# Kernel tuning notes

Hardware: AMD Instinct MI355X
Metric: run time of the kernel (lower is better)

Reference implementation:

```python
import jax, jax.numpy as jnp
import numpy as np

MAXDISP = 4  # matches init_kwargs


def setup_inputs() -> dict:
    key = jax.random.key(0)
    k1, k2 = jax.random.split(key)
    shape = (4, 64, 64, 128)  # (b, c, H, W)
    return {
        "refimg_fea": jax.random.normal(k1, shape, dtype=jnp.float32),
        "targetimg_fea": jax.random.normal(k2, shape, dtype=jnp.float32),
    }


def _correlation(ref, tgt, md=MAXDISP):
    # cost[b,c,i,j,y,x] = ref[b,c,y,x] * tgt[b,c,y+(j-md), x+(i-md)] when in
    # bounds, else 0 (the torch code pre-fills with zeros). Zero-padding the
    # target reproduces the out-of-bounds zeros exactly, since the product with
    # a padded zero is 0 and leaky_relu(0) == 0.
    b, c, H, W = ref.shape
    D = 2 * md + 1
    tpad = jnp.pad(tgt, ((0, 0), (0, 0), (md, md), (md, md)))

    def shift(i, j):
        # i indexes the width offset (ind), j the height offset (indd),
        # matching cost[:, :, i, j] in the original double loop.
        return jax.lax.dynamic_slice(tpad, (0, 0, j, i), (b, c, H, W))

    idx = jnp.arange(D)
    # shifts: [D_i, D_j, b, c, H, W]
    shifts = jax.vmap(lambda i: jax.vmap(lambda j: shift(i, j))(idx))(idx)
    cost = jax.nn.leaky_relu(ref[None, None] * shifts, negative_slope=0.1)
    # -> (b, c, D_i, D_j, H, W)
    return jnp.transpose(cost, (2, 3, 0, 1, 4, 5))


def reference(refimg_fea, targetimg_fea):
    return _correlation(refimg_fea, targetimg_fea, MAXDISP)
```

## Files before the change

kernel.cpp:

```cpp
#include <hip/hip_runtime.h>

#define MD 4
#define DD 9
#define B  4
#define C  64
#define H  64
#define W  128
#define W4 (W / 4)
#define HW (H * W)

typedef float f32x4 __attribute__((ext_vector_type(4)));


__device__ __forceinline__ float lrelu(float p) {
    return fmaxf(p, 0.1f * p);
}

__global__ __launch_bounds__(256) void corr_kernel(const float* __restrict__ ref,
                                                   const float* __restrict__ tgt,
                                                   float* __restrict__ out) {
    const unsigned bc = blockIdx.x >> 3;
    const unsigned yg = blockIdx.x & 7;
    const unsigned x4 = threadIdx.x & 31;
    const unsigned y  = yg * 8 + (threadIdx.x >> 5);
    const unsigned x  = x4 * 4;

    const f32x4 r = *reinterpret_cast<const f32x4*>(ref + ((size_t)bc * H + y) * W + x);

    float* const out_base = out + (size_t)bc * (DD * DD * HW) + (size_t)y * W + x;
    const float* const tgt_bc = tgt + (size_t)bc * HW;

    #pragma unroll
    for (int j = 0; j < DD; ++j) {
        const int ty = (int)y + j - MD;
        f32x4 tm = {0.f, 0.f, 0.f, 0.f};
        f32x4 tc = {0.f, 0.f, 0.f, 0.f};
        f32x4 tp = {0.f, 0.f, 0.f, 0.f};
        if (ty >= 0 && ty < H) {
            const float* trow = tgt_bc + (size_t)ty * W;
            if (x4 > 0)  tm = *reinterpret_cast<const f32x4*>(trow + x - 4);
            tc = *reinterpret_cast<const f32x4*>(trow + x);
            if (x4 < W4 - 1) tp = *reinterpret_cast<const f32x4*>(trow + x + 4);
        }
        float t[12] = {tm.x, tm.y, tm.z, tm.w,
                       tc.x, tc.y, tc.z, tc.w,
                       tp.x, tp.y, tp.z, tp.w};

        float* op = out_base + (size_t)j * HW;
        #pragma unroll
        for (int i = 0; i < DD; ++i) {
            f32x4 o;
            o.x = lrelu(r.x * t[i + 0]);
            o.y = lrelu(r.y * t[i + 1]);
            o.z = lrelu(r.z * t[i + 2]);
            o.w = lrelu(r.w * t[i + 3]);
            __builtin_nontemporal_store(o, reinterpret_cast<f32x4*>(op));
            op += (size_t)DD * HW;
        }
    }
}

extern "C" void kernel_launch(void* const* d_in, const int* in_sizes, int n_in,
                              void* d_out, int out_size, void* d_ws, size_t ws_size,
                              hipStream_t stream) {
    const float* ref = (const float*)d_in[0];
    const float* tgt = (const float*)d_in[1];
    float* out = (float*)d_out;

    const unsigned blocks = B * C * (H / 8);
    corr_kernel<<<blocks, 256, 0, stream>>>(ref, tgt, out);
}
```

Before: 136.7 us.

## Stage padded target plane in LDS and loop over width offsets per block

Each block now handles one (batch, channel) plane for three width offsets, loading the target plane into a zero-padded LDS tile per offset and reading shifted windows from LDS instead of issuing bounds-checked global loads. Reference rows are held in registers across all offsets. Grid shrinks to 768 blocks, with repeated LDS clearing and barriers between phases, which may reduce parallelism and the overlap of output stores in a write-bound kernel.

```diff
diff --git a/kernel.cpp b/kernel.cpp
--- a/kernel.cpp
+++ b/kernel.cpp
@@ -6,56 +6,84 @@
 #define C  64
 #define H  64
 #define W  128
-#define W4 (W / 4)
 #define HW (H * W)
+
+#define LROW  136
+#define LROWS 72
+#define LDS_F (LROWS * LROW)
 
 typedef float f32x4 __attribute__((ext_vector_type(4)));
 
-
-__device__ __forceinline__ float lrelu(float p) {
-    return fmaxf(p, 0.1f * p);
+__device__ __forceinline__ f32x4 lrelu4(f32x4 p) {
+    f32x4 o;
+    o.x = fmaxf(p.x, 0.1f * p.x);
+    o.y = fmaxf(p.y, 0.1f * p.y);
+    o.z = fmaxf(p.z, 0.1f * p.z);
+    o.w = fmaxf(p.w, 0.1f * p.w);
+    return o;
 }
 
 __global__ __launch_bounds__(256) void corr_kernel(const float* __restrict__ ref,
                                                    const float* __restrict__ tgt,
                                                    float* __restrict__ out) {
-    const unsigned bc = blockIdx.x >> 3;
-    const unsigned yg = blockIdx.x & 7;
-    const unsigned x4 = threadIdx.x & 31;
-    const unsigned y  = yg * 8 + (threadIdx.x >> 5);
-    const unsigned x  = x4 * 4;
+    __shared__ __align__(16) float ldsT[LDS_F];
 
-    const f32x4 r = *reinterpret_cast<const f32x4*>(ref + ((size_t)bc * H + y) * W + x);
+    const unsigned t  = threadIdx.x;
+    const unsigned bc = blockIdx.x / 3u;
+    const unsigned i0 = (blockIdx.x % 3u) * 3u;
+    const unsigned x4 = t & 31u;
+    const unsigned x  = x4 * 4u;
+    const unsigned yw = t >> 5;
 
-    float* const out_base = out + (size_t)bc * (DD * DD * HW) + (size_t)y * W + x;
-    const float* const tgt_bc = tgt + (size_t)bc * HW;
+    const float* refp = ref + (size_t)bc * HW;
+    const float* tgtp = tgt + (size_t)bc * HW;
 
+    f32x4 r8[8];
     #pragma unroll
-    for (int j = 0; j < DD; ++j) {
-        const int ty = (int)y + j - MD;
-        f32x4 tm = {0.f, 0.f, 0.f, 0.f};
-        f32x4 tc = {0.f, 0.f, 0.f, 0.f};
-        f32x4 tp = {0.f, 0.f, 0.f, 0.f};
-        if (ty >= 0 && ty < H) {
-            const float* trow = tgt_bc + (size_t)ty * W;
-            if (x4 > 0)  tm = *reinterpret_cast<const f32x4*>(trow + x - 4);
-            tc = *reinterpret_cast<const f32x4*>(trow + x);
-            if (x4 < W4 - 1) tp = *reinterpret_cast<const f32x4*>(trow + x + 4);
+    for (int s = 0; s < 8; ++s)
+        r8[s] = *reinterpret_cast<const f32x4*>(refp + (size_t)(s * 8 + yw) * W + x);
+
+    for (unsigned k = 0; k < 3; ++k) {
+        const unsigned i  = i0 + k;
+        const unsigned sh = 8u - i;
+
+        __syncthreads();
+
+        #pragma unroll
+        for (int z = 0; z < 10; ++z) {
+            unsigned idx = (unsigned)z * 256u + t;
+            if (idx < LDS_F / 4)
+                reinterpret_cast<f32x4*>(ldsT)[idx] = (f32x4){0.f, 0.f, 0.f, 0.f};
         }
-        float t[12] = {tm.x, tm.y, tm.z, tm.w,
-                       tc.x, tc.y, tc.z, tc.w,
-                       tp.x, tp.y, tp.z, tp.w};
+        __syncthreads();
 
-        float* op = out_base + (size_t)j * HW;
         #pragma unroll
-        for (int i = 0; i < DD; ++i) {
-            f32x4 o;
-            o.x = lrelu(r.x * t[i + 0]);
-            o.y = lrelu(r.y * t[i + 1]);
-            o.z = lrelu(r.z * t[i + 2]);
-            o.w = lrelu(r.w * t[i + 3]);
-            __builtin_nontemporal_store(o, reinterpret_cast<f32x4*>(op));
-            op += (size_t)DD * HW;
+        for (int z = 0; z < 8; ++z) {
+            unsigned idx = (unsigned)z * 256u + t;
+            unsigned row = idx >> 5;
+            unsigned c4  = idx & 31u;
+            f32x4 g = *reinterpret_cast<const f32x4*>(tgtp + (size_t)idx * 4u);
+            unsigned base = (row + MD) * LROW + c4 * 4u + sh;
+            ldsT[base + 0] = g.x;
+            ldsT[base + 1] = g.y;
+            ldsT[base + 2] = g.z;
+            ldsT[base + 3] = g.w;
+        }
+        __syncthreads();
+
+        float* outu = out + ((size_t)bc * (DD * DD) + (size_t)i * DD) * HW;
+        #pragma unroll
+        for (int j = 0; j < DD; ++j) {
+            float* oj = outu + (size_t)j * HW;
+            #pragma unroll
+            for (int s = 0; s < 8; ++s) {
+                const unsigned y = (unsigned)s * 8u + yw;
+                const f32x4 w = *reinterpret_cast<const f32x4*>(
+                    &ldsT[(y + (unsigned)j) * LROW + x + 4u]);
+                __builtin_nontemporal_store(
+                    lrelu4(r8[s] * w),
+                    reinterpret_cast<f32x4*>(oj + (size_t)y * W + x));
+            }
         }
     }
 }
@@ -67,6 +95,5 @@
     const float* tgt = (const float*)d_in[1];
     float* out = (float*)d_out;
 
-    const unsigned blocks = B * C * (H / 8);
-    corr_kernel<<<blocks, 256, 0, stream>>>(ref, tgt, out);
+    corr_kernel<<<768, 256, 0, stream>>>(ref, tgt, out);
 }
```

After: 148.1 us. +8.3%, slower.
